# Performance work log

Hardware: AMD Instinct MI355X
Metric: run time of the kernel (lower is better)

The kernel has to match this reference:

```python
import jax, jax.numpy as jnp
import numpy as np

N = 40000   # nodes
E = 600000  # edges
F = 128     # feature/hidden dim
G = 64      # graphs in batch


def setup_inputs() -> dict:
    key = jax.random.key(0)
    ks = jax.random.split(key, 16)
    x = jax.random.normal(ks[0], (N, F), dtype=jnp.float32)
    src = jax.random.randint(ks[1], (E,), 0, N)
    dst = jax.random.randint(ks[2], (E,), 0, N)
    edge_index = jnp.stack([src, dst]).astype(jnp.int64)
    batch = jnp.sort(jax.random.randint(ks[3], (N,), 0, G)).astype(jnp.int64)
    s = 1.0 / np.sqrt(F)
    W0 = jax.random.normal(ks[4], (F, F), dtype=jnp.float32) * s
    b0 = jnp.zeros((F,), dtype=jnp.float32)
    W1 = jax.random.normal(ks[5], (F, F), dtype=jnp.float32) * s
    b1 = jnp.zeros((F,), dtype=jnp.float32)
    W2 = jax.random.normal(ks[6], (F, F), dtype=jnp.float32) * s
    b2 = jnp.zeros((F,), dtype=jnp.float32)
    lin_w = jax.random.normal(ks[7], (F, 1), dtype=jnp.float32) * s
    lin_b = jnp.zeros((1,), dtype=jnp.float32)
    return {"x": x, "edge_index": edge_index, "batch": batch,
            "W0": W0, "b0": b0, "W1": W1, "b1": b1, "W2": W2, "b2": b2,
            "lin_w": lin_w, "lin_b": lin_b}


def _gcn_conv(x, W, b, src, dst, norm, num_nodes):
    # PyG GCNConv: linear transform, gather source, normalize, scatter-add to dst, add bias
    h = x @ W                                  # [N, F_out]
    msg = h[src] * norm[:, None]               # [E+N, F_out]
    agg = jax.ops.segment_sum(msg, dst, num_segments=num_nodes)
    return agg + b


def reference(x, edge_index, batch, W0, b0, W1, b1, W2, b2, lin_w, lin_b):
    num_nodes = x.shape[0]
    loops = jnp.arange(num_nodes, dtype=edge_index.dtype)
    src = jnp.concatenate([edge_index[0], loops])   # add self-loops
    dst = jnp.concatenate([edge_index[1], loops])
    # symmetric normalization deg^-1/2 (degree over in-edges incl. self loops)
    deg = jax.ops.segment_sum(jnp.ones_like(src, dtype=x.dtype), dst,
                              num_segments=num_nodes)
    dinv = jnp.where(deg > 0, jax.lax.rsqrt(jnp.maximum(deg, 1e-12)), 0.0)
    norm = dinv[src] * dinv[dst]                    # [E+N]

    h = jax.nn.relu(_gcn_conv(x, W0, b0, src, dst, norm, num_nodes))
    h = jax.nn.relu(_gcn_conv(h, W1, b1, src, dst, norm, num_nodes))
    h = jax.nn.relu(_gcn_conv(h, W2, b2, src, dst, norm, num_nodes))

    # global_mean_pool over ragged graph segments
    sums = jax.ops.segment_sum(h, batch, num_segments=G)            # [G, F]
    counts = jax.ops.segment_sum(jnp.ones((num_nodes,), h.dtype), batch,
                                 num_segments=G)                    # [G]
    pooled = sums / jnp.maximum(counts, 1.0)[:, None]
    return pooled @ lin_w + lin_b                                   # [G, 1]
```

## Files before the change

### kernel.cpp

```cpp
#include <hip/hip_runtime.h>
#include <hip/hip_bf16.h>

#define F_DIM 128
#define POOL_SEG 16

typedef __attribute__((ext_vector_type(8))) short short8v;
typedef __attribute__((ext_vector_type(4))) float float4v;


__device__ __forceinline__ ushort f2bf(float f) {
    uint u = __float_as_uint(f);
    u += 0x7fffu + ((u >> 16) & 1u);
    return (ushort)(u >> 16);
}
__device__ __forceinline__ float bf2f(ushort h) {
    return __uint_as_float(((uint)h) << 16);
}
__device__ __forceinline__ void bf2x(uint u, float& a, float& b) {
    a = __uint_as_float((u & 0x0000ffffu) << 16);
    b = __uint_as_float(u & 0xffff0000u);
}


__global__ void count_kernel(const int* __restrict__ dst, int* __restrict__ deg, int E_) {
    int i = blockIdx.x * blockDim.x + threadIdx.x;
    if (i < E_) atomicAdd(&deg[dst[i]], 1);
}

__global__ void scan_blocksums_kernel(const int* __restrict__ deg, int* __restrict__ bsum, int N_) {
    __shared__ int s[256];
    int i = blockIdx.x * 256 + threadIdx.x;
    s[threadIdx.x] = (i < N_) ? deg[i] : 0;
    __syncthreads();
    for (int off = 128; off; off >>= 1) {
        if (threadIdx.x < off) s[threadIdx.x] += s[threadIdx.x + off];
        __syncthreads();
    }
    if (threadIdx.x == 0) bsum[blockIdx.x] = s[0];
}

__global__ void scan_bs_kernel(const int* __restrict__ bsum, int* __restrict__ bsx, int NB) {
    __shared__ int s[256];
    int t = threadIdx.x;
    int orig = (t < NB) ? bsum[t] : 0;
    s[t] = orig;
    __syncthreads();
    for (int off = 1; off < 256; off <<= 1) {
        int v = (t >= off) ? s[t - off] : 0;
        __syncthreads();
        s[t] += v;
        __syncthreads();
    }
    if (t < NB) bsx[t] = s[t] - orig;
}

__global__ void scan_final_kernel(const int* __restrict__ deg, const int* __restrict__ bsx,
                                  int* __restrict__ row_ptr, int* __restrict__ rfill,
                                  float* __restrict__ dinv, int N_, int E_) {
    __shared__ int s[256];
    int t = threadIdx.x;
    int i = blockIdx.x * 256 + t;
    int orig = (i < N_) ? deg[i] : 0;
    s[t] = orig;
    __syncthreads();
    for (int off = 1; off < 256; off <<= 1) {
        int v = (t >= off) ? s[t - off] : 0;
        __syncthreads();
        s[t] += v;
        __syncthreads();
    }
    int excl = s[t] - orig + bsx[blockIdx.x];
    if (i < N_) {
        row_ptr[i] = excl;
        rfill[i] = excl;
        dinv[i] = 1.0f / sqrtf((float)(orig + 1));
    }
    if (i == N_ - 1) row_ptr[N_] = E_;
}

__global__ void fill_kernel(const int* __restrict__ src, const int* __restrict__ dst,
                            int* __restrict__ cur, int* __restrict__ col_src, int E_) {
    int i = blockIdx.x * blockDim.x + threadIdx.x;
    if (i < E_) {
        int p = atomicAdd(&cur[dst[i]], 1);
        col_src[p] = src[i];
    }
}


__global__ __launch_bounds__(256) void prep_kernel(
    const float* __restrict__ W0, const float* __restrict__ W1, const float* __restrict__ W2,
    ushort* __restrict__ Wth, ushort* __restrict__ Wtl, int* __restrict__ deg, int N_)
{
    if (blockIdx.x >= 48) {
        int i = (blockIdx.x - 48) * 256 + threadIdx.x;
        if (i < N_) deg[i] = 0;
        return;
    }
    int layer = blockIdx.x >> 4;
    int chunkc = blockIdx.x & 15;
    const float* W = (layer == 0) ? W0 : (layer == 1) ? W1 : W2;
    int t = threadIdx.x;
    int c  = chunkc * 8 + (t >> 5);
    int k0 = (t & 31) * 4;
    ushort4 hi, lo;
    float v0 = W[(size_t)(k0 + 0) * F_DIM + c];
    float v1 = W[(size_t)(k0 + 1) * F_DIM + c];
    float v2 = W[(size_t)(k0 + 2) * F_DIM + c];
    float v3 = W[(size_t)(k0 + 3) * F_DIM + c];
    hi.x = f2bf(v0); lo.x = f2bf(v0 - bf2f(hi.x));
    hi.y = f2bf(v1); lo.y = f2bf(v1 - bf2f(hi.y));
    hi.z = f2bf(v2); lo.z = f2bf(v2 - bf2f(hi.z));
    hi.w = f2bf(v3); lo.w = f2bf(v3 - bf2f(hi.w));
    size_t o = (size_t)layer * F_DIM * F_DIM + (size_t)c * F_DIM + k0;
    *reinterpret_cast<ushort4*>(&Wth[o]) = hi;
    *reinterpret_cast<ushort4*>(&Wtl[o]) = lo;
}


__global__ __launch_bounds__(256) void gemm_scale_kernel(
    const float* __restrict__ in, const ushort* __restrict__ Wth, const ushort* __restrict__ Wtl,
    const float* __restrict__ dinv, ushort* __restrict__ outbf, int N_)
{
    __shared__ ushort Ah[64 * F_DIM];
    __shared__ ushort Al[64 * F_DIM];
    __shared__ ushort Bh[64 * F_DIM];
    __shared__ ushort Bl[64 * F_DIM];

    const int tid = threadIdx.x;
    const int brow = (blockIdx.x >> 1) * 64;
    const int bcol = (blockIdx.x & 1) * 64;

    #pragma unroll
    for (int i = 0; i < 4; ++i) {
        int chunk = tid + i * 256;
        int r  = chunk >> 4;
        int k0 = (chunk & 15) * 8;
        int row = brow + r;
        float f[8];
        if (row < N_) {
            float4 g0 = *reinterpret_cast<const float4*>(&in[(size_t)row * F_DIM + k0]);
            float4 g1 = *reinterpret_cast<const float4*>(&in[(size_t)row * F_DIM + k0 + 4]);
            f[0] = g0.x; f[1] = g0.y; f[2] = g0.z; f[3] = g0.w;
            f[4] = g1.x; f[5] = g1.y; f[6] = g1.z; f[7] = g1.w;
        } else {
            #pragma unroll
            for (int j = 0; j < 8; ++j) f[j] = 0.f;
        }
        ushort hi[8], lo[8];
        #pragma unroll
        for (int j = 0; j < 8; ++j) {
            hi[j] = f2bf(f[j]);
            lo[j] = f2bf(f[j] - bf2f(hi[j]));
        }
        int idx = r * F_DIM + (k0 ^ ((r & 7) << 3));
        *reinterpret_cast<short8v*>(&Ah[idx]) = *reinterpret_cast<short8v*>(hi);
        *reinterpret_cast<short8v*>(&Al[idx]) = *reinterpret_cast<short8v*>(lo);
    }
    #pragma unroll
    for (int i = 0; i < 4; ++i) {
        int chunk = tid + i * 256;
        int c  = chunk >> 4;
        int k0 = (chunk & 15) * 8;
        size_t go = (size_t)(bcol + c) * F_DIM + k0;
        int idx = c * F_DIM + (k0 ^ ((c & 7) << 3));
        *reinterpret_cast<short8v*>(&Bh[idx]) = *reinterpret_cast<const short8v*>(&Wth[go]);
        *reinterpret_cast<short8v*>(&Bl[idx]) = *reinterpret_cast<const short8v*>(&Wtl[go]);
    }
    __syncthreads();

    const int l = tid & 63;
    const int wave = tid >> 6;
    const int m0 = wave * 16;
    const int row_a = m0 + (l & 15);
    const int kgrp = (l >> 4) * 8;
    const int aswz = (row_a & 7) << 3;

    float4v acc[4] = {{0.f,0.f,0.f,0.f},{0.f,0.f,0.f,0.f},{0.f,0.f,0.f,0.f},{0.f,0.f,0.f,0.f}};

    #pragma unroll
    for (int kk = 0; kk < 4; ++kk) {
        int kbase = kk * 32 + kgrp;
        short8v a_h = *reinterpret_cast<short8v*>(&Ah[row_a * F_DIM + (kbase ^ aswz)]);
        short8v a_l = *reinterpret_cast<short8v*>(&Al[row_a * F_DIM + (kbase ^ aswz)]);
        #pragma unroll
        for (int n = 0; n < 4; ++n) {
            int col_b = n * 16 + (l & 15);
            int bidx = col_b * F_DIM + (kbase ^ ((col_b & 7) << 3));
            short8v b_h = *reinterpret_cast<short8v*>(&Bh[bidx]);
            short8v b_l = *reinterpret_cast<short8v*>(&Bl[bidx]);
            acc[n] = __builtin_amdgcn_mfma_f32_16x16x32_bf16(a_h, b_h, acc[n], 0, 0, 0);
            acc[n] = __builtin_amdgcn_mfma_f32_16x16x32_bf16(a_l, b_h, acc[n], 0, 0, 0);
            acc[n] = __builtin_amdgcn_mfma_f32_16x16x32_bf16(a_h, b_l, acc[n], 0, 0, 0);
        }
    }

    #pragma unroll
    for (int i = 0; i < 4; ++i) {
        int rloc = m0 + (l >> 4) * 4 + i;
        int row = brow + rloc;
        if (row < N_) {
            float s = dinv[row];
            #pragma unroll
            for (int n = 0; n < 4; ++n) {
                ushort o = f2bf(s * acc[n][i]);
                outbf[(size_t)row * F_DIM + bcol + n * 16 + (l & 15)] = o;
            }
        }
    }
}


__global__ __launch_bounds__(256) void gather_kernel(
    const ushort* __restrict__ Mbf, const int* __restrict__ row_ptr,
    const int* __restrict__ col_src, const float* __restrict__ dinv,
    const float* __restrict__ bias, float* __restrict__ Hout, int N_)
{
    int v = blockIdx.x * 4 + (threadIdx.x >> 6);
    if (v >= N_) return;
    const int lane = threadIdx.x & 63;
    const int fq  = lane & 15;
    const int sub = lane >> 4;
    const uint4* M4 = reinterpret_cast<const uint4*>(Mbf);

    float acc[8];
    #pragma unroll
    for (int j = 0; j < 8; ++j) acc[j] = 0.f;

    int lo = row_ptr[v];
    int total = row_ptr[v + 1] - lo + 1;

    for (int base = 0; base < total; base += 64) {
        int nidx = total - base; if (nidx > 64) nidx = 64;
        int p = base + lane;
        int idx = v;
        if (p > 0 && p < total) idx = col_src[lo + p - 1];

        int nslots = (nidx + 3) >> 2;
        int jfull  = (nidx >> 4) * 4;
        int j = 0;
        for (; j < jfull; j += 4) {
            int q0 = j * 4 + sub;
            int s0 = __shfl(idx, q0);
            int s1 = __shfl(idx, q0 + 4);
            int s2 = __shfl(idx, q0 + 8);
            int s3 = __shfl(idx, q0 + 12);
            uint4 u0 = M4[(size_t)s0 * 16 + fq];
            uint4 u1 = M4[(size_t)s1 * 16 + fq];
            uint4 u2 = M4[(size_t)s2 * 16 + fq];
            uint4 u3 = M4[(size_t)s3 * 16 + fq];
            float a, b;
            bf2x(u0.x, a, b); acc[0] += a; acc[1] += b;
            bf2x(u0.y, a, b); acc[2] += a; acc[3] += b;
            bf2x(u0.z, a, b); acc[4] += a; acc[5] += b;
            bf2x(u0.w, a, b); acc[6] += a; acc[7] += b;
            bf2x(u1.x, a, b); acc[0] += a; acc[1] += b;
            bf2x(u1.y, a, b); acc[2] += a; acc[3] += b;
            bf2x(u1.z, a, b); acc[4] += a; acc[5] += b;
            bf2x(u1.w, a, b); acc[6] += a; acc[7] += b;
            bf2x(u2.x, a, b); acc[0] += a; acc[1] += b;
            bf2x(u2.y, a, b); acc[2] += a; acc[3] += b;
            bf2x(u2.z, a, b); acc[4] += a; acc[5] += b;
            bf2x(u2.w, a, b); acc[6] += a; acc[7] += b;
            bf2x(u3.x, a, b); acc[0] += a; acc[1] += b;
            bf2x(u3.y, a, b); acc[2] += a; acc[3] += b;
            bf2x(u3.z, a, b); acc[4] += a; acc[5] += b;
            bf2x(u3.w, a, b); acc[6] += a; acc[7] += b;
        }
        if (j < nslots) {
            int q0 = j * 4 + sub;
            int q1 = q0 + 4, q2 = q0 + 8, q3 = q0 + 12;
            int c0 = min(q0, nidx - 1), c1 = min(q1, nidx - 1);
            int c2 = min(q2, nidx - 1), c3 = min(q3, nidx - 1);
            int s0 = __shfl(idx, c0);
            int s1 = __shfl(idx, c1);
            int s2 = __shfl(idx, c2);
            int s3 = __shfl(idx, c3);
            float m0 = (q0 < nidx) ? 1.f : 0.f;
            float m1 = (q1 < nidx) ? 1.f : 0.f;
            float m2 = (q2 < nidx) ? 1.f : 0.f;
            float m3 = (q3 < nidx) ? 1.f : 0.f;
            uint4 u0 = M4[(size_t)s0 * 16 + fq];
            uint4 u1 = M4[(size_t)s1 * 16 + fq];
            uint4 u2 = M4[(size_t)s2 * 16 + fq];
            uint4 u3 = M4[(size_t)s3 * 16 + fq];
            float a, b;
            bf2x(u0.x, a, b); acc[0] = fmaf(a, m0, acc[0]); acc[1] = fmaf(b, m0, acc[1]);
            bf2x(u0.y, a, b); acc[2] = fmaf(a, m0, acc[2]); acc[3] = fmaf(b, m0, acc[3]);
            bf2x(u0.z, a, b); acc[4] = fmaf(a, m0, acc[4]); acc[5] = fmaf(b, m0, acc[5]);
            bf2x(u0.w, a, b); acc[6] = fmaf(a, m0, acc[6]); acc[7] = fmaf(b, m0, acc[7]);
            bf2x(u1.x, a, b); acc[0] = fmaf(a, m1, acc[0]); acc[1] = fmaf(b, m1, acc[1]);
            bf2x(u1.y, a, b); acc[2] = fmaf(a, m1, acc[2]); acc[3] = fmaf(b, m1, acc[3]);
            bf2x(u1.z, a, b); acc[4] = fmaf(a, m1, acc[4]); acc[5] = fmaf(b, m1, acc[5]);
            bf2x(u1.w, a, b); acc[6] = fmaf(a, m1, acc[6]); acc[7] = fmaf(b, m1, acc[7]);
            bf2x(u2.x, a, b); acc[0] = fmaf(a, m2, acc[0]); acc[1] = fmaf(b, m2, acc[1]);
            bf2x(u2.y, a, b); acc[2] = fmaf(a, m2, acc[2]); acc[3] = fmaf(b, m2, acc[3]);
            bf2x(u2.z, a, b); acc[4] = fmaf(a, m2, acc[4]); acc[5] = fmaf(b, m2, acc[5]);
            bf2x(u2.w, a, b); acc[6] = fmaf(a, m2, acc[6]); acc[7] = fmaf(b, m2, acc[7]);
            bf2x(u3.x, a, b); acc[0] = fmaf(a, m3, acc[0]); acc[1] = fmaf(b, m3, acc[1]);
            bf2x(u3.y, a, b); acc[2] = fmaf(a, m3, acc[2]); acc[3] = fmaf(b, m3, acc[3]);
            bf2x(u3.z, a, b); acc[4] = fmaf(a, m3, acc[4]); acc[5] = fmaf(b, m3, acc[5]);
            bf2x(u3.w, a, b); acc[6] = fmaf(a, m3, acc[6]); acc[7] = fmaf(b, m3, acc[7]);
        }
    }

    #pragma unroll
    for (int j = 0; j < 8; ++j) {
        acc[j] += __shfl_xor(acc[j], 16);
        acc[j] += __shfl_xor(acc[j], 32);
    }

    if (sub == 0) {
        float dv = dinv[v];
        const float4* b4 = reinterpret_cast<const float4*>(bias);
        float4 bb0 = b4[fq * 2], bb1 = b4[fq * 2 + 1];
        float4 o0, o1;
        o0.x = fmaxf(dv * acc[0] + bb0.x, 0.0f);
        o0.y = fmaxf(dv * acc[1] + bb0.y, 0.0f);
        o0.z = fmaxf(dv * acc[2] + bb0.z, 0.0f);
        o0.w = fmaxf(dv * acc[3] + bb0.w, 0.0f);
        o1.x = fmaxf(dv * acc[4] + bb1.x, 0.0f);
        o1.y = fmaxf(dv * acc[5] + bb1.y, 0.0f);
        o1.z = fmaxf(dv * acc[6] + bb1.z, 0.0f);
        o1.w = fmaxf(dv * acc[7] + bb1.w, 0.0f);
        float4* H4 = reinterpret_cast<float4*>(&Hout[(size_t)v * F_DIM + fq * 8]);
        H4[0] = o0;
        H4[1] = o1;
    }
}


__device__ __forceinline__ int lower_bound_i(const int* __restrict__ a, int n, int key) {
    int lo = 0, hi = n;
    while (lo < hi) {
        int mid = (lo + hi) >> 1;
        if (a[mid] < key) lo = mid + 1; else hi = mid;
    }
    return lo;
}

__global__ __launch_bounds__(128) void pool_part_kernel(
    const float* __restrict__ H, const int* __restrict__ batch,
    float* __restrict__ partial, int N_)
{
    int g = blockIdx.x / POOL_SEG;
    int s = blockIdx.x % POOL_SEG;
    int lo = lower_bound_i(batch, N_, g);
    int hi = lower_bound_i(batch, N_, g + 1);
    int len = hi - lo;
    int chunk = (len + POOL_SEG - 1) / POOL_SEG;
    int a = lo + s * chunk;
    int b = min(a + chunk, hi);
    int col = threadIdx.x;
    float acc = 0.f;
    for (int n = a; n < b; ++n) acc += H[(size_t)n * F_DIM + col];
    partial[((size_t)g * POOL_SEG + s) * F_DIM + col] = acc;
}

__global__ __launch_bounds__(128) void pool_final_kernel(
    const float* __restrict__ partial, const int* __restrict__ batch,
    const float* __restrict__ lin_w, const float* __restrict__ lin_b,
    float* __restrict__ out, int N_)
{
    int g = blockIdx.x;
    int col = threadIdx.x;
    float acc = 0.f;
    #pragma unroll
    for (int s = 0; s < POOL_SEG; ++s)
        acc += partial[((size_t)g * POOL_SEG + s) * F_DIM + col];
    int lo = lower_bound_i(batch, N_, g);
    int hi = lower_bound_i(batch, N_, g + 1);
    float pooled = acc / fmaxf((float)(hi - lo), 1.0f);
    float v = pooled * lin_w[col];
    __shared__ float sm[128];
    sm[col] = v;
    __syncthreads();
    if (col < 64) {
        float t = sm[col] + sm[col + 64];
        for (int off = 32; off; off >>= 1) t += __shfl_down(t, off);
        if (col == 0) out[g] = t + lin_b[0];
    }
}


extern "C" void kernel_launch(void* const* d_in, const int* in_sizes, int n_in,
                              void* d_out, int out_size, void* d_ws, size_t ws_size,
                              hipStream_t stream) {
    const float* x     = (const float*)d_in[0];
    const int*   ei    = (const int*)d_in[1];
    const int*   batch = (const int*)d_in[2];
    const float* W0    = (const float*)d_in[3];
    const float* b0    = (const float*)d_in[4];
    const float* W1    = (const float*)d_in[5];
    const float* b1    = (const float*)d_in[6];
    const float* W2    = (const float*)d_in[7];
    const float* b2    = (const float*)d_in[8];
    const float* lin_w = (const float*)d_in[9];
    const float* lin_b = (const float*)d_in[10];

    const int N_ = in_sizes[2];
    const int E_ = in_sizes[1] / 2;
    const int G_ = out_size;
    const int* esrc = ei;
    const int* edst = ei + E_;

    char* p = reinterpret_cast<char*>(d_ws);
    ushort* Mbf = reinterpret_cast<ushort*>(p);        p += (size_t)N_ * F_DIM * sizeof(ushort);
    float*  Hbuf = reinterpret_cast<float*>(p);        p += (size_t)N_ * F_DIM * sizeof(float);
    float*  dinvp = reinterpret_cast<float*>(p);       p += (size_t)N_ * sizeof(float);
    int*    deg = reinterpret_cast<int*>(p);           p += (size_t)N_ * sizeof(int);
    int*    row_ptr = reinterpret_cast<int*>(p);       p += (size_t)(N_ + 4) * sizeof(int);
    int*    rfill = reinterpret_cast<int*>(p);         p += (size_t)N_ * sizeof(int);
    int*    col_src = reinterpret_cast<int*>(p);       p += (size_t)E_ * sizeof(int);
    ushort* Wth = reinterpret_cast<ushort*>(p);        p += (size_t)3 * F_DIM * F_DIM * sizeof(ushort);
    ushort* Wtl = reinterpret_cast<ushort*>(p);        p += (size_t)3 * F_DIM * F_DIM * sizeof(ushort);
    const int NB = (N_ + 255) / 256;
    int*    bsum = reinterpret_cast<int*>(p);          p += (size_t)NB * sizeof(int);
    int*    bsx = reinterpret_cast<int*>(p);
    float*  partial = reinterpret_cast<float*>(d_ws);

    int eb = (E_ + 255) / 256;
    prep_kernel<<<48 + NB, 256, 0, stream>>>(W0, W1, W2, Wth, Wtl, deg, N_);
    count_kernel<<<eb, 256, 0, stream>>>(edst, deg, E_);
    scan_blocksums_kernel<<<NB, 256, 0, stream>>>(deg, bsum, N_);
    scan_bs_kernel<<<1, 256, 0, stream>>>(bsum, bsx, NB);
    scan_final_kernel<<<NB, 256, 0, stream>>>(deg, bsx, row_ptr, rfill, dinvp, N_, E_);
    fill_kernel<<<eb, 256, 0, stream>>>(esrc, edst, rfill, col_src, E_);

    const int gemm_grid = ((N_ + 63) / 64) * 2;
    const int gat_grid  = (N_ + 3) / 4;

    const float* cur_in = x;
    const float* bias[3] = {b0, b1, b2};
    for (int l = 0; l < 3; ++l) {
        gemm_scale_kernel<<<gemm_grid, 256, 0, stream>>>(
            cur_in, Wth + (size_t)l * F_DIM * F_DIM, Wtl + (size_t)l * F_DIM * F_DIM,
            dinvp, Mbf, N_);
        gather_kernel<<<gat_grid, 256, 0, stream>>>(
            Mbf, row_ptr, col_src, dinvp, bias[l], Hbuf, N_);
        cur_in = Hbuf;
    }

    pool_part_kernel<<<G_ * POOL_SEG, 128, 0, stream>>>(Hbuf, batch, partial, N_);
    pool_final_kernel<<<G_, 128, 0, stream>>>(partial, batch, lin_w, lin_b, (float*)d_out, N_);
}
```

Before: 214.1 us.

## Merge CSR build stages into one persistent kernel with grid barriers

Replaces the six preprocessing launches (weight prep, degree count, three scan stages, fill) with a single kernel of NB blocks that uses atomic-counter grid barriers between phases. The pooling partial and final kernels are also merged, with the last-arriving block per graph doing the final reduction. The goal is to cut kernel launch overhead and idle gaps between launches. In exchange, the grid barrier relies on all 157 blocks being co-resident, the edge loops now use a grid-stride loop over fewer threads, and an extra memset launch is added.

```diff
diff --git a/kernel.cpp b/kernel.cpp
--- a/kernel.cpp
+++ b/kernel.cpp
@@ -21,100 +21,104 @@
     b = __uint_as_float(u & 0xffff0000u);
 }
 
-
-__global__ void count_kernel(const int* __restrict__ dst, int* __restrict__ deg, int E_) {
-    int i = blockIdx.x * blockDim.x + threadIdx.x;
-    if (i < E_) atomicAdd(&deg[dst[i]], 1);
-}
-
-__global__ void scan_blocksums_kernel(const int* __restrict__ deg, int* __restrict__ bsum, int N_) {
-    __shared__ int s[256];
-    int i = blockIdx.x * 256 + threadIdx.x;
-    s[threadIdx.x] = (i < N_) ? deg[i] : 0;
-    __syncthreads();
-    for (int off = 128; off; off >>= 1) {
-        if (threadIdx.x < off) s[threadIdx.x] += s[threadIdx.x + off];
+__device__ __forceinline__ void dev_barrier(int* counter, int nblocks) {
+    __syncthreads();
+    if (threadIdx.x == 0) {
+        __threadfence();
+        atomicAdd(counter, 1);
+        while (atomicAdd(counter, 0) < nblocks) { }
+        __threadfence();
+    }
+    __syncthreads();
+}
+
+
+__global__ __launch_bounds__(256) void csr_build_kernel(
+    const float* __restrict__ W0, const float* __restrict__ W1, const float* __restrict__ W2,
+    ushort* __restrict__ Wth, ushort* __restrict__ Wtl,
+    const int* __restrict__ esrc, const int* __restrict__ edst,
+    int* __restrict__ deg, int* __restrict__ row_ptr, int* __restrict__ rfill,
+    float* __restrict__ dinv, int* __restrict__ col_src,
+    int* __restrict__ bsum, int* __restrict__ bsx, int* __restrict__ counters,
+    int N_, int E_, int NB)
+{
+    __shared__ int sdeg[256];
+    __shared__ int sscan[256];
+    __shared__ int sbx;
+    const int t = threadIdx.x;
+    const int bid = blockIdx.x;
+    const int nthreads = NB * 256;
+    const int gidx = bid * 256 + t;
+
+    if (gidx < N_) deg[gidx] = 0;
+    if (bid < 48) {
+        int layer = bid >> 4;
+        int chunkc = bid & 15;
+        const float* W = (layer == 0) ? W0 : (layer == 1) ? W1 : W2;
+        int c  = chunkc * 8 + (t >> 5);
+        int k0 = (t & 31) * 4;
+        ushort4 hi, lo;
+        float v0 = W[(size_t)(k0 + 0) * F_DIM + c];
+        float v1 = W[(size_t)(k0 + 1) * F_DIM + c];
+        float v2 = W[(size_t)(k0 + 2) * F_DIM + c];
+        float v3 = W[(size_t)(k0 + 3) * F_DIM + c];
+        hi.x = f2bf(v0); lo.x = f2bf(v0 - bf2f(hi.x));
+        hi.y = f2bf(v1); lo.y = f2bf(v1 - bf2f(hi.y));
+        hi.z = f2bf(v2); lo.z = f2bf(v2 - bf2f(hi.z));
+        hi.w = f2bf(v3); lo.w = f2bf(v3 - bf2f(hi.w));
+        size_t o = (size_t)layer * F_DIM * F_DIM + (size_t)c * F_DIM + k0;
+        *reinterpret_cast<ushort4*>(&Wth[o]) = hi;
+        *reinterpret_cast<ushort4*>(&Wtl[o]) = lo;
+    }
+    dev_barrier(&counters[0], NB);
+
+    for (int e = gidx; e < E_; e += nthreads)
+        atomicAdd(&deg[edst[e]], 1);
+    dev_barrier(&counters[1], NB);
+
+    int d = (gidx < N_) ? atomicAdd(&deg[gidx], 0) : 0;
+    sdeg[t] = d;
+    sscan[t] = d;
+    __syncthreads();
+    for (int off = 1; off < 256; off <<= 1) {
+        int v = (t >= off) ? sscan[t - off] : 0;
         __syncthreads();
-    }
-    if (threadIdx.x == 0) bsum[blockIdx.x] = s[0];
-}
-
-__global__ void scan_bs_kernel(const int* __restrict__ bsum, int* __restrict__ bsx, int NB) {
-    __shared__ int s[256];
-    int t = threadIdx.x;
-    int orig = (t < NB) ? bsum[t] : 0;
-    s[t] = orig;
-    __syncthreads();
-    for (int off = 1; off < 256; off <<= 1) {
-        int v = (t >= off) ? s[t - off] : 0;
+        sscan[t] += v;
         __syncthreads();
-        s[t] += v;
+    }
+    int incl = sscan[t];
+    if (t == 255) atomicExch(&bsum[bid], incl);
+    dev_barrier(&counters[2], NB);
+
+    if (bid == 0) {
+        int orig = (t < NB) ? atomicAdd(&bsum[t], 0) : 0;
+        sscan[t] = orig;
         __syncthreads();
-    }
-    if (t < NB) bsx[t] = s[t] - orig;
-}
-
-__global__ void scan_final_kernel(const int* __restrict__ deg, const int* __restrict__ bsx,
-                                  int* __restrict__ row_ptr, int* __restrict__ rfill,
-                                  float* __restrict__ dinv, int N_, int E_) {
-    __shared__ int s[256];
-    int t = threadIdx.x;
-    int i = blockIdx.x * 256 + t;
-    int orig = (i < N_) ? deg[i] : 0;
-    s[t] = orig;
-    __syncthreads();
-    for (int off = 1; off < 256; off <<= 1) {
-        int v = (t >= off) ? s[t - off] : 0;
-        __syncthreads();
-        s[t] += v;
-        __syncthreads();
-    }
-    int excl = s[t] - orig + bsx[blockIdx.x];
-    if (i < N_) {
-        row_ptr[i] = excl;
-        rfill[i] = excl;
-        dinv[i] = 1.0f / sqrtf((float)(orig + 1));
-    }
-    if (i == N_ - 1) row_ptr[N_] = E_;
-}
-
-__global__ void fill_kernel(const int* __restrict__ src, const int* __restrict__ dst,
-                            int* __restrict__ cur, int* __restrict__ col_src, int E_) {
-    int i = blockIdx.x * blockDim.x + threadIdx.x;
-    if (i < E_) {
-        int p = atomicAdd(&cur[dst[i]], 1);
-        col_src[p] = src[i];
-    }
-}
-
-
-__global__ __launch_bounds__(256) void prep_kernel(
-    const float* __restrict__ W0, const float* __restrict__ W1, const float* __restrict__ W2,
-    ushort* __restrict__ Wth, ushort* __restrict__ Wtl, int* __restrict__ deg, int N_)
-{
-    if (blockIdx.x >= 48) {
-        int i = (blockIdx.x - 48) * 256 + threadIdx.x;
-        if (i < N_) deg[i] = 0;
-        return;
-    }
-    int layer = blockIdx.x >> 4;
-    int chunkc = blockIdx.x & 15;
-    const float* W = (layer == 0) ? W0 : (layer == 1) ? W1 : W2;
-    int t = threadIdx.x;
-    int c  = chunkc * 8 + (t >> 5);
-    int k0 = (t & 31) * 4;
-    ushort4 hi, lo;
-    float v0 = W[(size_t)(k0 + 0) * F_DIM + c];
-    float v1 = W[(size_t)(k0 + 1) * F_DIM + c];
-    float v2 = W[(size_t)(k0 + 2) * F_DIM + c];
-    float v3 = W[(size_t)(k0 + 3) * F_DIM + c];
-    hi.x = f2bf(v0); lo.x = f2bf(v0 - bf2f(hi.x));
-    hi.y = f2bf(v1); lo.y = f2bf(v1 - bf2f(hi.y));
-    hi.z = f2bf(v2); lo.z = f2bf(v2 - bf2f(hi.z));
-    hi.w = f2bf(v3); lo.w = f2bf(v3 - bf2f(hi.w));
-    size_t o = (size_t)layer * F_DIM * F_DIM + (size_t)c * F_DIM + k0;
-    *reinterpret_cast<ushort4*>(&Wth[o]) = hi;
-    *reinterpret_cast<ushort4*>(&Wtl[o]) = lo;
+        for (int off = 1; off < 256; off <<= 1) {
+            int v = (t >= off) ? sscan[t - off] : 0;
+            __syncthreads();
+            sscan[t] += v;
+            __syncthreads();
+        }
+        if (t < NB) atomicExch(&bsx[t], sscan[t] - orig);
+    }
+    dev_barrier(&counters[3], NB);
+
+    if (t == 0) sbx = atomicAdd(&bsx[bid], 0);
+    __syncthreads();
+    int excl = incl - sdeg[t] + sbx;
+    if (gidx < N_) {
+        row_ptr[gidx] = excl;
+        atomicExch(&rfill[gidx], excl);
+        dinv[gidx] = 1.0f / sqrtf((float)(sdeg[t] + 1));
+    }
+    if (gidx == N_ - 1) row_ptr[N_] = E_;
+    dev_barrier(&counters[4], NB);
+
+    for (int e = gidx; e < E_; e += nthreads) {
+        int p = atomicAdd(&rfill[edst[e]], 1);
+        col_src[p] = esrc[e];
+    }
 }
 
 
@@ -339,9 +343,11 @@
     return lo;
 }
 
-__global__ __launch_bounds__(128) void pool_part_kernel(
+__global__ __launch_bounds__(128) void pool_kernel(
     const float* __restrict__ H, const int* __restrict__ batch,
-    float* __restrict__ partial, int N_)
+    const float* __restrict__ lin_w, const float* __restrict__ lin_b,
+    float* __restrict__ partial, int* __restrict__ pcount,
+    float* __restrict__ out, int N_)
 {
     int g = blockIdx.x / POOL_SEG;
     int s = blockIdx.x % POOL_SEG;
@@ -355,30 +361,28 @@
     float acc = 0.f;
     for (int n = a; n < b; ++n) acc += H[(size_t)n * F_DIM + col];
     partial[((size_t)g * POOL_SEG + s) * F_DIM + col] = acc;
-}
-
-__global__ __launch_bounds__(128) void pool_final_kernel(
-    const float* __restrict__ partial, const int* __restrict__ batch,
-    const float* __restrict__ lin_w, const float* __restrict__ lin_b,
-    float* __restrict__ out, int N_)
-{
-    int g = blockIdx.x;
-    int col = threadIdx.x;
-    float acc = 0.f;
-    #pragma unroll
-    for (int s = 0; s < POOL_SEG; ++s)
-        acc += partial[((size_t)g * POOL_SEG + s) * F_DIM + col];
-    int lo = lower_bound_i(batch, N_, g);
-    int hi = lower_bound_i(batch, N_, g + 1);
-    float pooled = acc / fmaxf((float)(hi - lo), 1.0f);
-    float v = pooled * lin_w[col];
-    __shared__ float sm[128];
-    sm[col] = v;
-    __syncthreads();
-    if (col < 64) {
-        float t = sm[col] + sm[col + 64];
-        for (int off = 32; off; off >>= 1) t += __shfl_down(t, off);
-        if (col == 0) out[g] = t + lin_b[0];
+    __threadfence();
+    __syncthreads();
+
+    __shared__ int sprev;
+    if (col == 0) sprev = atomicAdd(&pcount[g], 1);
+    __syncthreads();
+    if (sprev == POOL_SEG - 1) {
+        __threadfence();
+        float tot = 0.f;
+        #pragma unroll
+        for (int ss = 0; ss < POOL_SEG; ++ss)
+            tot += atomicAdd(&partial[((size_t)g * POOL_SEG + ss) * F_DIM + col], 0.0f);
+        float pooled = tot / fmaxf((float)len, 1.0f);
+        float v = pooled * lin_w[col];
+        __shared__ float sm[128];
+        sm[col] = v;
+        __syncthreads();
+        if (col < 64) {
+            float tt = sm[col] + sm[col + 64];
+            for (int off = 32; off; off >>= 1) tt += __shfl_down(tt, off);
+            if (col == 0) out[g] = tt + lin_b[0];
+        }
     }
 }
 
@@ -416,16 +420,16 @@
     ushort* Wtl = reinterpret_cast<ushort*>(p);        p += (size_t)3 * F_DIM * F_DIM * sizeof(ushort);
     const int NB = (N_ + 255) / 256;
     int*    bsum = reinterpret_cast<int*>(p);          p += (size_t)NB * sizeof(int);
-    int*    bsx = reinterpret_cast<int*>(p);
+    int*    bsx = reinterpret_cast<int*>(p);           p += (size_t)NB * sizeof(int);
+    int*    counters = reinterpret_cast<int*>(p);      p += 8 * sizeof(int);
+    int*    pcount = reinterpret_cast<int*>(p);        p += (size_t)G_ * sizeof(int);
     float*  partial = reinterpret_cast<float*>(d_ws);
 
-    int eb = (E_ + 255) / 256;
-    prep_kernel<<<48 + NB, 256, 0, stream>>>(W0, W1, W2, Wth, Wtl, deg, N_);
-    count_kernel<<<eb, 256, 0, stream>>>(edst, deg, E_);
-    scan_blocksums_kernel<<<NB, 256, 0, stream>>>(deg, bsum, N_);
-    scan_bs_kernel<<<1, 256, 0, stream>>>(bsum, bsx, NB);
-    scan_final_kernel<<<NB, 256, 0, stream>>>(deg, bsx, row_ptr, rfill, dinvp, N_, E_);
-    fill_kernel<<<eb, 256, 0, stream>>>(esrc, edst, rfill, col_src, E_);
+    hipMemsetAsync(counters, 0, (8 + (size_t)G_) * sizeof(int), stream);
+
+    csr_build_kernel<<<NB, 256, 0, stream>>>(
+        W0, W1, W2, Wth, Wtl, esrc, edst,
+        deg, row_ptr, rfill, dinvp, col_src, bsum, bsx, counters, N_, E_, NB);
 
     const int gemm_grid = ((N_ + 63) / 64) * 2;
     const int gat_grid  = (N_ + 3) / 4;
@@ -441,6 +445,6 @@
         cur_in = Hbuf;
     }
 
-    pool_part_kernel<<<G_ * POOL_SEG, 128, 0, stream>>>(Hbuf, batch, partial, N_);
-    pool_final_kernel<<<G_, 128, 0, stream>>>(partial, batch, lin_w, lin_b, (float*)d_out, N_);
-}
+    pool_kernel<<<G_ * POOL_SEG, 128, 0, stream>>>(
+        Hbuf, batch, lin_w, lin_b, partial, pcount, (float*)d_out, N_);
+}
```

After: 307.1 us. +43.4%, slower.
